# Optimization experiments

Measured on AMD Instinct MI355X. Metric: run time of the kernel, lower is better.

## Reference

```python
import jax, jax.numpy as jnp
import numpy as np

K_SIZE = 5  # local patch size


def extract_patches(x, k):
    """im2col-style k x k patch extraction with SAME zero padding.
    x: [B,H,W,C] -> [B,H,W,k*k,C]"""
    B, H, W, C = x.shape
    pad = k // 2
    xp = jnp.pad(x, ((0, 0), (pad, pad), (pad, pad), (0, 0)))
    # loop over fixed k*k offsets (25), stacked along a new patch axis
    slices = [xp[:, i:i + H, j:j + W, :] for i in range(k) for j in range(k)]
    return jnp.stack(slices, axis=3)  # [B,H,W,k*k,C]


def setup_inputs() -> dict:
    key = jax.random.key(0)
    k1, k2, k3 = jax.random.split(key, 3)
    B, H, W, C, BIN = 2, 128, 128, 64, 64
    return {
        "main": jax.random.normal(k1, (B, H, W, C), dtype=jnp.float32),
        "ref": jax.random.normal(k2, (B, H, W, C), dtype=jnp.float32),
        "ref_value": jax.random.normal(k3, (B, H, W, BIN), dtype=jnp.float32),
    }


def reference(main, ref, ref_value):
    k = K_SIZE
    ref_stacked = extract_patches(ref, k)            # [B,H,W,k*k,C]
    ref_value_stacked = extract_patches(ref_value, k)  # [B,H,W,k*k,BIN]
    # dot-product attention over the k*k patch axis
    scores = jnp.einsum('bhwpc,bhwc->bhwp', ref_stacked, main)  # [B,H,W,k*k]
    attn = jax.nn.softmax(scores, axis=3)
    # attention-weighted sum of value patches
    out = jnp.einsum('bhwp,bhwpv->bhwv', attn, ref_value_stacked)  # [B,H,W,BIN]
    return out
```

## Files before the change

kernel.cpp:

```cpp
#include <hip/hip_runtime.h>


#define BB 2
#define HH 128
#define WW 128
#define CC 64
#define KK 5
#define PAD 2
#define TC 20
#define NV (KK * TC)

template <int CTRL>
__device__ __forceinline__ float dpp_add(float v) {
    int r = __builtin_amdgcn_update_dpp(0, __float_as_int(v), CTRL, 0xF, 0xF, true);
    return v + __int_as_float(r);
}

__device__ __forceinline__ float group16_sum(float v) {
    v = dpp_add<0xB1>(v);
    v = dpp_add<0x4E>(v);
    v = dpp_add<0x124>(v);
    v = dpp_add<0x128>(v);
    return v;
}

__global__ __launch_bounds__(256, 4) void local_attn_kernel(
    const float* __restrict__ mainp,
    const float* __restrict__ refp,
    const float* __restrict__ refvp,
    float* __restrict__ outp)
{
    __shared__ float reft[NV * CC];

    const int tid    = threadIdx.x;
    const int lane16 = tid & 15;
    const int pix    = tid >> 4;
    const int seg    = blockIdx.x;
    const int wseg   = seg & 7;
    const int h      = (seg >> 3) & (HH - 1);
    const int b      = seg >> 10;
    const int w0     = wseg * 16;
    const int w      = w0 + pix;
    const int cb     = lane16 * 4;

    const size_t pbase = (((size_t)(b * HH + h)) * WW + w) * CC + cb;
    const float4 m4 = *reinterpret_cast<const float4*>(mainp + pbase);

    const bool interior = (wseg >= 1) & (wseg <= 6) & (h >= PAD) & (h < HH - PAD);

    {
        int r = 0, c = pix;
        if (interior) {
            const float* srcb =
                refp + (((size_t)(b * HH + h - PAD)) * WW + (w0 - PAD)) * CC + cb;
            #pragma unroll
            for (int i = 0; i < 7; ++i) {
                const int v = pix + 16 * i;
                if (v < NV) {
                    const float4 d = *reinterpret_cast<const float4*>(
                        srcb + ((size_t)(r * WW + c)) * CC);
                    *reinterpret_cast<float4*>(reft + (size_t)v * CC + cb) = d;
                }
                c += 16; const bool wr = (c >= TC); c = wr ? c - TC : c; r += wr;
            }
        } else {
            #pragma unroll
            for (int i = 0; i < 7; ++i) {
                const int v = pix + 16 * i;
                if (v < NV) {
                    const int hg  = h + r - PAD;
                    const int wg  = w0 + c - PAD;
                    const int hgc = min(max(hg, 0), HH - 1);
                    const int wgc = min(max(wg, 0), WW - 1);
                    const float4 d = *reinterpret_cast<const float4*>(
                        refp + (((size_t)(b * HH + hgc)) * WW + wgc) * CC + cb);
                    const bool ok = ((unsigned)hg < (unsigned)HH) &
                                    ((unsigned)wg < (unsigned)WW);
                    float4 z;
                    z.x = ok ? d.x : 0.0f;
                    z.y = ok ? d.y : 0.0f;
                    z.z = ok ? d.z : 0.0f;
                    z.w = ok ? d.w : 0.0f;
                    *reinterpret_cast<float4*>(reft + (size_t)v * CC + cb) = z;
                }
                c += 16; const bool wr = (c >= TC); c = wr ? c - TC : c; r += wr;
            }
        }
    }
    __syncthreads();

    const float* tbase = reft + pix * CC + cb;
    float sc[KK * KK];
    #pragma unroll
    for (int r = 0; r < KK; ++r) {
        #pragma unroll
        for (int dj = 0; dj < KK; ++dj) {
            const float4 t =
                *reinterpret_cast<const float4*>(tbase + (r * TC + dj) * CC);
            sc[r * KK + dj] = m4.x * t.x + m4.y * t.y + m4.z * t.z + m4.w * t.w;
        }
    }

    #pragma unroll
    for (int p = 0; p < KK * KK; ++p) sc[p] = group16_sum(sc[p]);

    float mx = sc[0];
    #pragma unroll
    for (int p = 1; p < KK * KK; ++p) mx = fmaxf(mx, sc[p]);
    float ssum = 0.0f;
    #pragma unroll
    for (int p = 0; p < KK * KK; ++p) { sc[p] = __expf(sc[p] - mx); ssum += sc[p]; }
    const float inv = 1.0f / ssum;

    float4 acc = make_float4(0.f, 0.f, 0.f, 0.f);
    if (interior) {
        const float* vb = refvp + pbase;
        #pragma unroll
        for (int di = 0; di < KK; ++di) {
            const float* row = vb + (ptrdiff_t)(di - PAD) * (WW * CC);
            #pragma unroll
            for (int dj = 0; dj < KK; ++dj) {
                const float4 v4 =
                    *reinterpret_cast<const float4*>(row + (dj - PAD) * CC);
                const float a = sc[di * KK + dj];
                acc.x += a * v4.x;
                acc.y += a * v4.y;
                acc.z += a * v4.z;
                acc.w += a * v4.w;
            }
        }
    } else {
        int   wwc[KK];
        float wokf[KK];
        #pragma unroll
        for (int dj = 0; dj < KK; ++dj) {
            const int ww_ = w + dj - PAD;
            wwc[dj]  = min(max(ww_, 0), WW - 1);
            wokf[dj] = ((unsigned)ww_ < (unsigned)WW) ? 1.0f : 0.0f;
        }
        #pragma unroll
        for (int di = 0; di < KK; ++di) {
            const int hh_  = h + di - PAD;
            const int hhc  = min(max(hh_, 0), HH - 1);
            const float hokf = ((unsigned)hh_ < (unsigned)HH) ? 1.0f : 0.0f;
            const float* row = refvp + (((size_t)(b * HH + hhc)) * WW) * CC + cb;
            #pragma unroll
            for (int dj = 0; dj < KK; ++dj) {
                const float4 v4 =
                    *reinterpret_cast<const float4*>(row + (size_t)wwc[dj] * CC);
                const float a = sc[di * KK + dj] * hokf * wokf[dj];
                acc.x += a * v4.x;
                acc.y += a * v4.y;
                acc.z += a * v4.z;
                acc.w += a * v4.w;
            }
        }
    }
    acc.x *= inv; acc.y *= inv; acc.z *= inv; acc.w *= inv;

    *reinterpret_cast<float4*>(outp + pbase) = acc;
}

extern "C" void kernel_launch(void* const* d_in, const int* in_sizes, int n_in,
                              void* d_out, int out_size, void* d_ws, size_t ws_size,
                              hipStream_t stream) {
    const float* mainp = (const float*)d_in[0];
    const float* refp  = (const float*)d_in[1];
    const float* refvp = (const float*)d_in[2];
    float* outp        = (float*)d_out;

    const int blocks = BB * HH * (WW / 16);
    local_attn_kernel<<<blocks, 256, 0, stream>>>(mainp, refp, refvp, outp);
}
```

Baseline: 85.48 us.

## Stage ref and value tiles into LDS via direct global-to-LDS loads

The value tile is now staged into shared memory alongside the ref tile. Both use the global_load_lds builtin, which writes straight into LDS without going through registers, so the 25 value reads per pixel come from LDS instead of overlapping global loads. This doubles LDS use per block and lowers the launch-bounds occupancy hint from 4 to 3. It also relies on the asynchronous LDS loads being complete at the existing barrier, and on the per-wave address mapping (v0base) matching the layout the compute phase expects.

```diff
diff --git a/kernel.cpp b/kernel.cpp
--- a/kernel.cpp
+++ b/kernel.cpp
@@ -1,4 +1,5 @@
 #include <hip/hip_runtime.h>
+#include <cstdint>
 
 
 #define BB 2
@@ -24,13 +25,21 @@
     return v;
 }
 
-__global__ __launch_bounds__(256, 4) void local_attn_kernel(
+__device__ __forceinline__ void lds_load16(const float* g, float* l) {
+    __builtin_amdgcn_global_load_lds(
+        (const __attribute__((address_space(1))) void*)(uintptr_t)g,
+        (__attribute__((address_space(3))) void*)(uint32_t)(uintptr_t)l,
+        16, 0, 0);
+}
+
+__global__ __launch_bounds__(256, 3) void local_attn_kernel(
     const float* __restrict__ mainp,
     const float* __restrict__ refp,
     const float* __restrict__ refvp,
     float* __restrict__ outp)
 {
     __shared__ float reft[NV * CC];
+    __shared__ float valt[NV * CC];
 
     const int tid    = threadIdx.x;
     const int lane16 = tid & 15;
@@ -47,33 +56,38 @@
     const float4 m4 = *reinterpret_cast<const float4*>(mainp + pbase);
 
     const bool interior = (wseg >= 1) & (wseg <= 6) & (h >= PAD) & (h < HH - PAD);
+    const int v0base = (tid >> 6) * 4;
 
     {
         int r = 0, c = pix;
         if (interior) {
-            const float* srcb =
-                refp + (((size_t)(b * HH + h - PAD)) * WW + (w0 - PAD)) * CC + cb;
+            const size_t obase =
+                (((size_t)(b * HH + h - PAD)) * WW + (w0 - PAD)) * CC + cb;
             #pragma unroll
             for (int i = 0; i < 7; ++i) {
-                const int v = pix + 16 * i;
-                if (v < NV) {
-                    const float4 d = *reinterpret_cast<const float4*>(
-                        srcb + ((size_t)(r * WW + c)) * CC);
-                    *reinterpret_cast<float4*>(reft + (size_t)v * CC + cb) = d;
+                const int v0 = v0base + 16 * i;
+                if (v0 < NV) {
+                    const size_t off = obase + ((size_t)(r * WW + c)) * CC;
+                    lds_load16(refp  + off, reft + (size_t)v0 * CC);
+                    lds_load16(refvp + off, valt + (size_t)v0 * CC);
                 }
                 c += 16; const bool wr = (c >= TC); c = wr ? c - TC : c; r += wr;
             }
         } else {
             #pragma unroll
             for (int i = 0; i < 7; ++i) {
-                const int v = pix + 16 * i;
-                if (v < NV) {
+                const int v0 = v0base + 16 * i;
+                if (v0 < NV) {
+                    const int v   = pix + 16 * i;
                     const int hg  = h + r - PAD;
                     const int wg  = w0 + c - PAD;
                     const int hgc = min(max(hg, 0), HH - 1);
                     const int wgc = min(max(wg, 0), WW - 1);
-                    const float4 d = *reinterpret_cast<const float4*>(
-                        refp + (((size_t)(b * HH + hgc)) * WW + wgc) * CC + cb);
+                    const size_t coff =
+                        (((size_t)(b * HH + hgc)) * WW + wgc) * CC + cb;
+                    lds_load16(refvp + coff, valt + (size_t)v0 * CC);
+                    const float4 d =
+                        *reinterpret_cast<const float4*>(refp + coff);
                     const bool ok = ((unsigned)hg < (unsigned)HH) &
                                     ((unsigned)wg < (unsigned)WW);
                     float4 z;
@@ -112,16 +126,15 @@
     for (int p = 0; p < KK * KK; ++p) { sc[p] = __expf(sc[p] - mx); ssum += sc[p]; }
     const float inv = 1.0f / ssum;
 
+    const float* vtb = valt + pix * CC + cb;
     float4 acc = make_float4(0.f, 0.f, 0.f, 0.f);
     if (interior) {
-        const float* vb = refvp + pbase;
         #pragma unroll
         for (int di = 0; di < KK; ++di) {
-            const float* row = vb + (ptrdiff_t)(di - PAD) * (WW * CC);
             #pragma unroll
             for (int dj = 0; dj < KK; ++dj) {
                 const float4 v4 =
-                    *reinterpret_cast<const float4*>(row + (dj - PAD) * CC);
+                    *reinterpret_cast<const float4*>(vtb + (di * TC + dj) * CC);
                 const float a = sc[di * KK + dj];
                 acc.x += a * v4.x;
                 acc.y += a * v4.y;
@@ -130,24 +143,20 @@
             }
         }
     } else {
-        int   wwc[KK];
         float wokf[KK];
         #pragma unroll
         for (int dj = 0; dj < KK; ++dj) {
             const int ww_ = w + dj - PAD;
-            wwc[dj]  = min(max(ww_, 0), WW - 1);
             wokf[dj] = ((unsigned)ww_ < (unsigned)WW) ? 1.0f : 0.0f;
         }
         #pragma unroll
         for (int di = 0; di < KK; ++di) {
-            const int hh_  = h + di - PAD;
-            const int hhc  = min(max(hh_, 0), HH - 1);
+            const int hh_   = h + di - PAD;
             const float hokf = ((unsigned)hh_ < (unsigned)HH) ? 1.0f : 0.0f;
-            const float* row = refvp + (((size_t)(b * HH + hhc)) * WW) * CC + cb;
             #pragma unroll
             for (int dj = 0; dj < KK; ++dj) {
                 const float4 v4 =
-                    *reinterpret_cast<const float4*>(row + (size_t)wwc[dj] * CC);
+                    *reinterpret_cast<const float4*>(vtb + (di * TC + dj) * CC);
                 const float a = sc[di * KK + dj] * hokf * wokf[dj];
                 acc.x += a * v4.x;
                 acc.y += a * v4.y;
```

Measured after the change: 84.67 us. About the same (-1.0%).
